# Optimization experiments

Hardware: AMD Instinct MI355X
Metric: run time of the kernel (lower is better)

## Reference

```python
import jax, jax.numpy as jnp
import numpy as np

NUM_HEADS = 12


def setup_inputs() -> dict:
    key = jax.random.key(0)
    k1, k2, k3 = jax.random.split(key, 3)
    B, S, D = 8, 1024, 768
    x = jax.random.normal(k1, (B, S, D), dtype=jnp.float32)
    # Linear weights, torch convention [out_features, in_features], small init
    w_qkv = jax.random.normal(k2, (3 * D, D), dtype=jnp.float32) * 0.02
    b_qkv = jnp.zeros((3 * D,), dtype=jnp.float32)
    w_proj = jax.random.normal(k3, (D, D), dtype=jnp.float32) * 0.02
    b_proj = jnp.zeros((D,), dtype=jnp.float32)
    return {"x": x, "w_qkv": w_qkv, "b_qkv": b_qkv, "w_proj": w_proj, "b_proj": b_proj}


def reference(x, w_qkv, b_qkv, w_proj, b_proj):
    B, S, D = x.shape
    H = NUM_HEADS
    hd = D // H
    qkv = x @ w_qkv.T + b_qkv                      # [B, S, 3D]
    qkv = qkv.reshape(B, S, 3, H, hd).transpose(2, 0, 3, 1, 4)  # [3, B, H, S, hd]
    q, k, v = qkv[0], qkv[1], qkv[2]
    # NOTE: source computes self.scale but never applies it -> unscaled QK^T
    weights = jnp.einsum('bhqd,bhkd->bhqk', q, k)  # [B, H, S, S]
    attn = jax.nn.softmax(weights, axis=-1)        # dropout = 0 (eval)
    out = jnp.einsum('bhqk,bhkd->bhqd', attn, v)   # [B, H, S, hd]
    out = out.transpose(0, 2, 1, 3).reshape(B, S, D)
    return out @ w_proj.T + b_proj
```

## Files before the change

kernel.cpp:

```cpp
#include <hip/hip_runtime.h>


typedef short bf16x8 __attribute__((ext_vector_type(8)));
typedef float f32x4  __attribute__((ext_vector_type(4)));

#define MFMA16(a, b, c) __builtin_amdgcn_mfma_f32_16x16x32_bf16((a), (b), (c), 0, 0, 0)

__device__ __forceinline__ unsigned short f2bf(float f) {
    union { float f; unsigned int u; } v; v.f = f;
    unsigned int u = v.u;
    return (unsigned short)((u + 0x7fffu + ((u >> 16) & 1u)) >> 16);
}

__device__ __forceinline__ unsigned int cvt2(float x, float y) {
#if __has_builtin(__builtin_amdgcn_cvt_pk_bf16_f32)
    auto v = __builtin_amdgcn_cvt_pk_bf16_f32(x, y);
    unsigned int b; __builtin_memcpy(&b, &v, 4); return b;
#else
    return (unsigned int)f2bf(x) | ((unsigned int)f2bf(y) << 16);
#endif
}

__device__ __forceinline__ void gl2lds16(const unsigned short* g, unsigned short* l) {
    __builtin_amdgcn_global_load_lds(
        (const unsigned int __attribute__((address_space(1)))*)g,
        (unsigned int __attribute__((address_space(3)))*)l,
        16, 0, 0);
}

__global__ void cvt3_kernel(const float* __restrict__ x,
                            const float* __restrict__ wq,
                            const float* __restrict__ wp,
                            unsigned short* __restrict__ xb,
                            unsigned short* __restrict__ wqb,
                            unsigned short* __restrict__ wpb) {
    int i = blockIdx.x * 256 + threadIdx.x;
    const float* s; unsigned short* d; int off;
    if (i < 1572864)      { s = x;  d = xb;  off = i; }
    else if (i < 2015232) { s = wq; d = wqb; off = i - 1572864; }
    else                  { s = wp; d = wpb; off = i - 2015232; }
    float4 v = ((const float4*)s)[off];
    ushort4 o;
    o.x = f2bf(v.x); o.y = f2bf(v.y); o.z = f2bf(v.z); o.w = f2bf(v.w);
    ((ushort4*)d)[off] = o;
}

__global__ __launch_bounds__(512, 4) void gemm_qkv(
    const unsigned short* __restrict__ A,
    const unsigned short* __restrict__ Bm,
    const float* __restrict__ bias,
    unsigned short* __restrict__ Qo,
    unsigned short* __restrict__ Ko,
    unsigned short* __restrict__ Vto) {
    const int K = 768;
    __shared__ __align__(16) unsigned short smem[16384];
    unsigned short* const As0 = smem;
    unsigned short* const As1 = smem + 4096;
    unsigned short* const Bs0 = smem + 8192;
    unsigned short* const Bs1 = smem + 12288;
    const int tid = threadIdx.x;
    const int wave = tid >> 6, lane = tid & 63;
    const int quad = lane >> 4, l16 = lane & 15;
    const int wm = (wave >> 1) * 32, wn = (wave & 1) * 64;
    const int tileM = blockIdx.x * 128, tileN = blockIdx.y * 128;

    f32x4 zero4 = {0.f, 0.f, 0.f, 0.f};
    f32x4 acc[2][4];
#pragma unroll
    for (int i = 0; i < 2; ++i)
#pragma unroll
        for (int j = 0; j < 4; ++j) acc[i][j] = zero4;

    const int sr = tid >> 2, sc = tid & 3;
    const unsigned short* Ag = A + (size_t)(tileM + sr) * K + sc * 8;
    const unsigned short* Bg = Bm + (size_t)(tileN + sr) * K + sc * 8;
    const int sdst = wave << 9;

    auto compute = [&](const unsigned short* Ar, const unsigned short* Br) {
        bf16x8 af[2], bfr[4];
#pragma unroll
        for (int t = 0; t < 2; ++t)
            af[t] = *(const bf16x8*)(Ar + (wm + t * 16 + l16) * 32 + quad * 8);
#pragma unroll
        for (int t = 0; t < 4; ++t)
            bfr[t] = *(const bf16x8*)(Br + (wn + t * 16 + l16) * 32 + quad * 8);
#pragma unroll
        for (int tm = 0; tm < 2; ++tm)
#pragma unroll
            for (int tn = 0; tn < 4; ++tn)
                acc[tm][tn] = MFMA16(af[tm], bfr[tn], acc[tm][tn]);
    };

    gl2lds16(Ag, As0 + sdst);
    gl2lds16(Bg, Bs0 + sdst);
    for (int it = 0; it < 24; it += 2) {
        __syncthreads();
        {
            int k1 = (it + 1) << 5;
            gl2lds16(Ag + k1, As1 + sdst);
            gl2lds16(Bg + k1, Bs1 + sdst);
        }
        compute(As0, Bs0);
        __syncthreads();
        if (it + 2 < 24) {
            int k2 = (it + 2) << 5;
            gl2lds16(Ag + k2, As0 + sdst);
            gl2lds16(Bg + k2, Bs0 + sdst);
        }
        compute(As1, Bs1);
    }

    const int t = blockIdx.y / 6;
    if (t < 2) {
        const float scale = (t == 0) ? 1.44269504f : 1.0f;
        unsigned short* dst = (t == 0) ? Qo : Ko;
        const int nb = tileN - t * 768 + wn;
#pragma unroll
        for (int tm = 0; tm < 2; ++tm) {
#pragma unroll
            for (int tn = 0; tn < 4; ++tn) {
                int nl = nb + tn * 16 + l16;
                float bv = bias[tileN + wn + tn * 16 + l16];
#pragma unroll
                for (int r = 0; r < 4; ++r) {
                    int m = tileM + wm + tm * 16 + quad * 4 + r;
                    dst[(size_t)m * 768 + nl] = f2bf((acc[tm][tn][r] + bv) * scale);
                }
            }
        }
    } else {
        const int b = tileM >> 10, srow = tileM & 1023;
#pragma unroll
        for (int h2 = 0; h2 < 2; ++h2) {
            __syncthreads();
            if ((wave & 1) == h2) {
#pragma unroll
                for (int tn = 0; tn < 4; ++tn) {
                    int dl = tn * 16 + l16;
                    float bv = bias[tileN + h2 * 64 + dl];
#pragma unroll
                    for (int tm = 0; tm < 2; ++tm) {
                        int mb = wm + tm * 16 + quad * 4;
                        uint2 pk;
                        pk.x = cvt2(acc[tm][tn][0] + bv, acc[tm][tn][1] + bv);
                        pk.y = cvt2(acc[tm][tn][2] + bv, acc[tm][tn][3] + bv);
                        *(uint2*)(smem + dl * 136 + mb) = pk;
                    }
                }
            }
            __syncthreads();
#pragma unroll
            for (int pass = 0; pass < 2; ++pass) {
                int dl = pass * 32 + (tid >> 4), soff = (tid & 15) * 8;
                bf16x8 row = *(const bf16x8*)(smem + dl * 136 + soff);
                int rem = tileN + h2 * 64 + dl - 1536;
                int h = rem >> 6, d = rem & 63;
                *(bf16x8*)(Vto + (((size_t)b * 12 + h) * 64 + d) * 1024 + srow + soff) = row;
            }
        }
    }
}

__global__ __launch_bounds__(256) void attn_kernel(
    const unsigned short* __restrict__ Q,
    const unsigned short* __restrict__ Kg,
    const unsigned short* __restrict__ Vt,
    unsigned short* __restrict__ O) {
    __shared__ __align__(16) unsigned short smem[24576];
    unsigned short* Ps = smem;

    const int tid = threadIdx.x;
    const int wave = tid >> 6, lane = tid & 63;
    const int quad = lane >> 4, l16 = lane & 15;
    const int s4 = l16 & 3;
    const int bh = blockIdx.x;
    const int qt = blockIdx.y;
    const int b = bh / 12, h = bh - b * 12;

    const unsigned short* Qb = Q  + ((size_t)b * 1024 + qt * 128) * 768 + h * 64;
    const unsigned short* Kb = Kg + (size_t)b * 1024 * 768 + h * 64;
    const unsigned short* Vb = Vt + (size_t)bh * 64 * 1024;

    auto stageKV = [&](int kv0, int buf) {
        int r = tid >> 2, c = tid & 3;
        const unsigned short* gk = Kb + (size_t)(kv0 + r) * 768 + c * 8;
        const unsigned short* gv = Vb + (size_t)r * 1024 + kv0 + c * 8;
        unsigned short* Kd = smem + 8192 + buf * 4096;
        unsigned short* Vd = smem + 16384 + buf * 4096;
        int dst = (wave << 6) * 8;
        gl2lds16(gk,      Kd + dst);
        gl2lds16(gk + 32, Kd + 2048 + dst);
        gl2lds16(gv,      Vd + dst);
        gl2lds16(gv + 32, Vd + 2048 + dst);
    };

#pragma unroll
    for (int i = 0; i < 2; ++i) {
        int s = tid + (i << 8);
        int r = s >> 2, c = s & 3;
        const unsigned short* gq = Qb + (size_t)r * 768 + c * 8;
        int dst = ((wave << 6) + (i << 8)) * 8;
        gl2lds16(gq,      smem + dst);
        gl2lds16(gq + 32, smem + 4096 + dst);
    }
    stageKV(0, 0);
    __syncthreads();
    bf16x8 qf[2][2];
#pragma unroll
    for (int ks = 0; ks < 2; ++ks)
#pragma unroll
        for (int tq = 0; tq < 2; ++tq)
            qf[ks][tq] = *(const bf16x8*)(smem + ks * 4096 +
                                          (wave * 32 + tq * 16 + l16) * 32 + quad * 8);
    __syncthreads();

    f32x4 zero4 = {0.f, 0.f, 0.f, 0.f};
    f32x4 oacc[2][4];
    float rsum[2] = {0.f, 0.f};
#pragma unroll
    for (int tm = 0; tm < 2; ++tm)
#pragma unroll
        for (int tv = 0; tv < 4; ++tv) oacc[tm][tv] = zero4;

    for (int it = 0; it < 16; ++it) {
        if (it + 1 < 16) stageKV((it + 1) << 6, (it + 1) & 1);
        const unsigned short* Kr = smem + 8192 + (it & 1) * 4096;
        const unsigned short* Vr = smem + 16384 + (it & 1) * 4096;

        f32x4 st[4][2];
#pragma unroll
        for (int tk = 0; tk < 4; ++tk)
#pragma unroll
            for (int tq = 0; tq < 2; ++tq) st[tk][tq] = zero4;
#pragma unroll
        for (int ks = 0; ks < 2; ++ks) {
            bf16x8 kf[4];
#pragma unroll
            for (int tk = 0; tk < 4; ++tk)
                kf[tk] = *(const bf16x8*)(Kr + ks * 2048 + (tk * 16 + l16) * 32 + quad * 8);
#pragma unroll
            for (int tk = 0; tk < 4; ++tk)
#pragma unroll
                for (int tq = 0; tq < 2; ++tq)
                    st[tk][tq] = MFMA16(kf[tk], qf[ks][tq], st[tk][tq]);
        }

#pragma unroll
        for (int tq = 0; tq < 2; ++tq) {
            unsigned short* prp = Ps + (wave * 32 + tq * 16 + l16) * 64 + quad * 4;
#pragma unroll
            for (int tk = 0; tk < 4; ++tk) {
                float e0 = __builtin_amdgcn_exp2f(st[tk][tq][0]);
                float e1 = __builtin_amdgcn_exp2f(st[tk][tq][1]);
                float e2 = __builtin_amdgcn_exp2f(st[tk][tq][2]);
                float e3 = __builtin_amdgcn_exp2f(st[tk][tq][3]);
                rsum[tq] += (e0 + e1) + (e2 + e3);
                uint2 pk;
                pk.x = cvt2(e0, e1);
                pk.y = cvt2(e2, e3);
                *(uint2*)(prp + ((tk ^ s4) << 4)) = pk;
            }
        }

#pragma unroll
        for (int ks2 = 0; ks2 < 2; ++ks2) {
            bf16x8 ap[2], bv[4];
            int colswz = ((ks2 << 5) + (quad << 3)) ^ (s4 << 4);
#pragma unroll
            for (int tm = 0; tm < 2; ++tm)
                ap[tm] = *(const bf16x8*)(Ps + (wave * 32 + tm * 16 + l16) * 64 + colswz);
#pragma unroll
            for (int tv = 0; tv < 4; ++tv)
                bv[tv] = *(const bf16x8*)(Vr + ks2 * 2048 + (tv * 16 + l16) * 32 + quad * 8);
#pragma unroll
            for (int tm = 0; tm < 2; ++tm)
#pragma unroll
                for (int tv = 0; tv < 4; ++tv)
                    oacc[tm][tv] = MFMA16(ap[tm], bv[tv], oacc[tm][tv]);
        }
        __syncthreads();
    }

#pragma unroll
    for (int tq = 0; tq < 2; ++tq) {
        rsum[tq] += __shfl_xor(rsum[tq], 16, 64);
        rsum[tq] += __shfl_xor(rsum[tq], 32, 64);
    }
    float* sums = (float*)smem;
    if (quad == 0) {
        sums[wave * 32 + l16]      = rsum[0];
        sums[wave * 32 + 16 + l16] = rsum[1];
    }
    __syncthreads();

#pragma unroll
    for (int tm = 0; tm < 2; ++tm) {
        f32x4 inv;
#pragma unroll
        for (int r = 0; r < 4; ++r)
            inv[r] = 1.0f / sums[wave * 32 + tm * 16 + quad * 4 + r];
#pragma unroll
        for (int tv = 0; tv < 4; ++tv)
#pragma unroll
            for (int r = 0; r < 4; ++r) {
                int srow = qt * 128 + wave * 32 + tm * 16 + quad * 4 + r;
                int col = h * 64 + tv * 16 + l16;
                O[((size_t)b * 1024 + srow) * 768 + col] = f2bf(oacc[tm][tv][r] * inv[r]);
            }
    }
}

__global__ __launch_bounds__(512, 4) void gemm_proj(
    const unsigned short* __restrict__ A,
    const unsigned short* __restrict__ Bm,
    const float* __restrict__ bias,
    float* __restrict__ out) {
    const int K = 768;
    __shared__ __align__(16) unsigned short smem[16384];
    unsigned short* const As0 = smem;
    unsigned short* const As1 = smem + 4096;
    unsigned short* const Bs0 = smem + 8192;
    unsigned short* const Bs1 = smem + 12288;
    const int tid = threadIdx.x;
    const int wave = tid >> 6, lane = tid & 63;
    const int quad = lane >> 4, l16 = lane & 15;
    const int wm = (wave >> 1) * 32, wn = (wave & 1) * 64;
    const int tileM = blockIdx.x * 128, tileN = blockIdx.y * 128;

    f32x4 zero4 = {0.f, 0.f, 0.f, 0.f};
    f32x4 acc[2][4];
#pragma unroll
    for (int i = 0; i < 2; ++i)
#pragma unroll
        for (int j = 0; j < 4; ++j) acc[i][j] = zero4;

    const int sr = tid >> 2, sc = tid & 3;
    const unsigned short* Ag = A + (size_t)(tileM + sr) * K + sc * 8;
    const unsigned short* Bg = Bm + (size_t)(tileN + sr) * K + sc * 8;
    const int sdst = wave << 9;

    auto compute = [&](const unsigned short* Ar, const unsigned short* Br) {
        bf16x8 af[2], bfr[4];
#pragma unroll
        for (int t = 0; t < 2; ++t)
            af[t] = *(const bf16x8*)(Ar + (wm + t * 16 + l16) * 32 + quad * 8);
#pragma unroll
        for (int t = 0; t < 4; ++t)
            bfr[t] = *(const bf16x8*)(Br + (wn + t * 16 + l16) * 32 + quad * 8);
#pragma unroll
        for (int tm = 0; tm < 2; ++tm)
#pragma unroll
            for (int tn = 0; tn < 4; ++tn)
                acc[tm][tn] = MFMA16(af[tm], bfr[tn], acc[tm][tn]);
    };

    gl2lds16(Ag, As0 + sdst);
    gl2lds16(Bg, Bs0 + sdst);
    for (int it = 0; it < 24; it += 2) {
        __syncthreads();
        {
            int k1 = (it + 1) << 5;
            gl2lds16(Ag + k1, As1 + sdst);
            gl2lds16(Bg + k1, Bs1 + sdst);
        }
        compute(As0, Bs0);
        __syncthreads();
        if (it + 2 < 24) {
            int k2 = (it + 2) << 5;
            gl2lds16(Ag + k2, As0 + sdst);
            gl2lds16(Bg + k2, Bs0 + sdst);
        }
        compute(As1, Bs1);
    }

#pragma unroll
    for (int tm = 0; tm < 2; ++tm) {
#pragma unroll
        for (int tn = 0; tn < 4; ++tn) {
            int n = tileN + wn + tn * 16 + l16;
            float bv = bias[n];
#pragma unroll
            for (int r = 0; r < 4; ++r) {
                int m = tileM + wm + tm * 16 + quad * 4 + r;
                out[(size_t)m * 768 + n] = acc[tm][tn][r] + bv;
            }
        }
    }
}

extern "C" void kernel_launch(void* const* d_in, const int* in_sizes, int n_in,
                              void* d_out, int out_size, void* d_ws, size_t ws_size,
                              hipStream_t stream) {
    (void)in_sizes; (void)n_in; (void)out_size; (void)ws_size;
    const float* x      = (const float*)d_in[0];
    const float* w_qkv  = (const float*)d_in[1];
    const float* b_qkv  = (const float*)d_in[2];
    const float* w_proj = (const float*)d_in[3];
    const float* b_proj = (const float*)d_in[4];
    float* out = (float*)d_out;

    char* ws = (char*)d_ws;
    unsigned short* xb     = (unsigned short*)(ws + 0);
    unsigned short* wqkvb  = (unsigned short*)(ws + 12582912);
    unsigned short* wprojb = (unsigned short*)(ws + 16121856);
    unsigned short* Qw     = (unsigned short*)(ws + 17301504);
    unsigned short* Kw     = (unsigned short*)(ws + 29884416);
    unsigned short* Vtw    = (unsigned short*)(ws + 42467328);

    cvt3_kernel<<<8448, 256, 0, stream>>>(x, w_qkv, w_proj, xb, wqkvb, wprojb);
    gemm_qkv<<<dim3(64, 18), 512, 0, stream>>>(xb, wqkvb, b_qkv, Qw, Kw, Vtw);
    attn_kernel<<<dim3(96, 8), 256, 0, stream>>>(Qw, Kw, Vtw, xb);
    gemm_proj<<<dim3(64, 6), 512, 0, stream>>>(xb, wprojb, b_proj, out);
}
```

Before: 187.0 us.

## Halve attention query tile to 64 rows and use MFMA-fragment-ordered LDS layout

```diff
diff --git a/kernel.cpp b/kernel.cpp
--- a/kernel.cpp
+++ b/kernel.cpp
@@ -161,153 +161,115 @@
     }
 }
 
-__global__ __launch_bounds__(256) void attn_kernel(
+__global__ __launch_bounds__(256, 4) void attn_kernel(
     const unsigned short* __restrict__ Q,
     const unsigned short* __restrict__ Kg,
     const unsigned short* __restrict__ Vt,
     unsigned short* __restrict__ O) {
-    __shared__ __align__(16) unsigned short smem[24576];
-    unsigned short* Ps = smem;
+    __shared__ __align__(16) unsigned short smem[20480];
 
     const int tid = threadIdx.x;
     const int wave = tid >> 6, lane = tid & 63;
     const int quad = lane >> 4, l16 = lane & 15;
-    const int s4 = l16 & 3;
     const int bh = blockIdx.x;
     const int qt = blockIdx.y;
     const int b = bh / 12, h = bh - b * 12;
 
-    const unsigned short* Qb = Q  + ((size_t)b * 1024 + qt * 128) * 768 + h * 64;
+    const unsigned short* Qb = Q  + ((size_t)b * 1024 + qt * 64) * 768 + h * 64;
     const unsigned short* Kb = Kg + (size_t)b * 1024 * 768 + h * 64;
     const unsigned short* Vb = Vt + (size_t)bh * 64 * 1024;
 
+    const int c0 = wave * 2, c1 = c0 + 1;
+    const unsigned short* gk0 = Kb + (size_t)((c0 & 3) * 16 + l16) * 768 + (c0 >> 2) * 32 + quad * 8;
+    const unsigned short* gk1 = Kb + (size_t)((c1 & 3) * 16 + l16) * 768 + (c1 >> 2) * 32 + quad * 8;
+    const unsigned short* gv0 = Vb + (size_t)((c0 & 3) * 16 + l16) * 1024 + (c0 >> 2) * 32 + quad * 8;
+    const unsigned short* gv1 = Vb + (size_t)((c1 & 3) * 16 + l16) * 1024 + (c1 >> 2) * 32 + quad * 8;
+
     auto stageKV = [&](int kv0, int buf) {
-        int r = tid >> 2, c = tid & 3;
-        const unsigned short* gk = Kb + (size_t)(kv0 + r) * 768 + c * 8;
-        const unsigned short* gv = Vb + (size_t)r * 1024 + kv0 + c * 8;
-        unsigned short* Kd = smem + 8192 + buf * 4096;
-        unsigned short* Vd = smem + 16384 + buf * 4096;
-        int dst = (wave << 6) * 8;
-        gl2lds16(gk,      Kd + dst);
-        gl2lds16(gk + 32, Kd + 2048 + dst);
-        gl2lds16(gv,      Vd + dst);
-        gl2lds16(gv + 32, Vd + 2048 + dst);
+        unsigned short* Kd = smem + 4096 + buf * 4096;
+        unsigned short* Vd = smem + 12288 + buf * 4096;
+        gl2lds16(gk0 + (size_t)kv0 * 768, Kd + c0 * 512);
+        gl2lds16(gk1 + (size_t)kv0 * 768, Kd + c1 * 512);
+        gl2lds16(gv0 + kv0, Vd + c0 * 512);
+        gl2lds16(gv1 + kv0, Vd + c1 * 512);
     };
 
-#pragma unroll
-    for (int i = 0; i < 2; ++i) {
-        int s = tid + (i << 8);
-        int r = s >> 2, c = s & 3;
-        const unsigned short* gq = Qb + (size_t)r * 768 + c * 8;
-        int dst = ((wave << 6) + (i << 8)) * 8;
-        gl2lds16(gq,      smem + dst);
-        gl2lds16(gq + 32, smem + 4096 + dst);
-    }
+    gl2lds16(Qb + (size_t)(wave * 16 + l16) * 768 + quad * 8,      smem + c0 * 512);
+    gl2lds16(Qb + (size_t)(wave * 16 + l16) * 768 + 32 + quad * 8, smem + c1 * 512);
     stageKV(0, 0);
     __syncthreads();
-    bf16x8 qf[2][2];
-#pragma unroll
-    for (int ks = 0; ks < 2; ++ks)
-#pragma unroll
-        for (int tq = 0; tq < 2; ++tq)
-            qf[ks][tq] = *(const bf16x8*)(smem + ks * 4096 +
-                                          (wave * 32 + tq * 16 + l16) * 32 + quad * 8);
-    __syncthreads();
-
+    bf16x8 qf[2];
+    qf[0] = *(const bf16x8*)(smem + c0 * 512 + lane * 8);
+    qf[1] = *(const bf16x8*)(smem + c1 * 512 + lane * 8);
+
+    unsigned short* Pw = smem + wave * 1024;
     f32x4 zero4 = {0.f, 0.f, 0.f, 0.f};
-    f32x4 oacc[2][4];
-    float rsum[2] = {0.f, 0.f};
-#pragma unroll
-    for (int tm = 0; tm < 2; ++tm)
-#pragma unroll
-        for (int tv = 0; tv < 4; ++tv) oacc[tm][tv] = zero4;
+    f32x4 oacc[4];
+    float rsum = 0.f;
+#pragma unroll
+    for (int tv = 0; tv < 4; ++tv) oacc[tv] = zero4;
 
     for (int it = 0; it < 16; ++it) {
         if (it + 1 < 16) stageKV((it + 1) << 6, (it + 1) & 1);
-        const unsigned short* Kr = smem + 8192 + (it & 1) * 4096;
-        const unsigned short* Vr = smem + 16384 + (it & 1) * 4096;
-
-        f32x4 st[4][2];
-#pragma unroll
-        for (int tk = 0; tk < 4; ++tk)
-#pragma unroll
-            for (int tq = 0; tq < 2; ++tq) st[tk][tq] = zero4;
+        const unsigned short* Kr = smem + 4096 + (it & 1) * 4096;
+        const unsigned short* Vr = smem + 12288 + (it & 1) * 4096;
+
+        f32x4 st[4];
+#pragma unroll
+        for (int tk = 0; tk < 4; ++tk) st[tk] = zero4;
 #pragma unroll
         for (int ks = 0; ks < 2; ++ks) {
             bf16x8 kf[4];
 #pragma unroll
             for (int tk = 0; tk < 4; ++tk)
-                kf[tk] = *(const bf16x8*)(Kr + ks * 2048 + (tk * 16 + l16) * 32 + quad * 8);
+                kf[tk] = *(const bf16x8*)(Kr + (ks * 4 + tk) * 512 + lane * 8);
 #pragma unroll
             for (int tk = 0; tk < 4; ++tk)
-#pragma unroll
-                for (int tq = 0; tq < 2; ++tq)
-                    st[tk][tq] = MFMA16(kf[tk], qf[ks][tq], st[tk][tq]);
-        }
-
-#pragma unroll
-        for (int tq = 0; tq < 2; ++tq) {
-            unsigned short* prp = Ps + (wave * 32 + tq * 16 + l16) * 64 + quad * 4;
-#pragma unroll
-            for (int tk = 0; tk < 4; ++tk) {
-                float e0 = __builtin_amdgcn_exp2f(st[tk][tq][0]);
-                float e1 = __builtin_amdgcn_exp2f(st[tk][tq][1]);
-                float e2 = __builtin_amdgcn_exp2f(st[tk][tq][2]);
-                float e3 = __builtin_amdgcn_exp2f(st[tk][tq][3]);
-                rsum[tq] += (e0 + e1) + (e2 + e3);
-                uint2 pk;
-                pk.x = cvt2(e0, e1);
-                pk.y = cvt2(e2, e3);
-                *(uint2*)(prp + ((tk ^ s4) << 4)) = pk;
-            }
+                st[tk] = MFMA16(kf[tk], qf[ks], st[tk]);
+        }
+
+#pragma unroll
+        for (int tk = 0; tk < 4; ++tk) {
+            float e0 = __builtin_amdgcn_exp2f(st[tk][0]);
+            float e1 = __builtin_amdgcn_exp2f(st[tk][1]);
+            float e2 = __builtin_amdgcn_exp2f(st[tk][2]);
+            float e3 = __builtin_amdgcn_exp2f(st[tk][3]);
+            rsum += (e0 + e1) + (e2 + e3);
+            uint2 pk;
+            pk.x = cvt2(e0, e1);
+            pk.y = cvt2(e2, e3);
+            *(uint2*)(Pw + (tk * 2 + (quad >> 1)) * 128 + l16 * 8 + (quad & 1) * 4) = pk;
         }
 
 #pragma unroll
         for (int ks2 = 0; ks2 < 2; ++ks2) {
-            bf16x8 ap[2], bv[4];
-            int colswz = ((ks2 << 5) + (quad << 3)) ^ (s4 << 4);
-#pragma unroll
-            for (int tm = 0; tm < 2; ++tm)
-                ap[tm] = *(const bf16x8*)(Ps + (wave * 32 + tm * 16 + l16) * 64 + colswz);
+            bf16x8 ap = *(const bf16x8*)(Pw + ks2 * 512 + lane * 8);
+            bf16x8 bv[4];
 #pragma unroll
             for (int tv = 0; tv < 4; ++tv)
-                bv[tv] = *(const bf16x8*)(Vr + ks2 * 2048 + (tv * 16 + l16) * 32 + quad * 8);
-#pragma unroll
-            for (int tm = 0; tm < 2; ++tm)
-#pragma unroll
-                for (int tv = 0; tv < 4; ++tv)
-                    oacc[tm][tv] = MFMA16(ap[tm], bv[tv], oacc[tm][tv]);
-        }
-        __syncthreads();
-    }
-
-#pragma unroll
-    for (int tq = 0; tq < 2; ++tq) {
-        rsum[tq] += __shfl_xor(rsum[tq], 16, 64);
-        rsum[tq] += __shfl_xor(rsum[tq], 32, 64);
-    }
-    float* sums = (float*)smem;
-    if (quad == 0) {
-        sums[wave * 32 + l16]      = rsum[0];
-        sums[wave * 32 + 16 + l16] = rsum[1];
-    }
-    __syncthreads();
-
-#pragma unroll
-    for (int tm = 0; tm < 2; ++tm) {
-        f32x4 inv;
-#pragma unroll
-        for (int r = 0; r < 4; ++r)
-            inv[r] = 1.0f / sums[wave * 32 + tm * 16 + quad * 4 + r];
-#pragma unroll
-        for (int tv = 0; tv < 4; ++tv)
-#pragma unroll
-            for (int r = 0; r < 4; ++r) {
-                int srow = qt * 128 + wave * 32 + tm * 16 + quad * 4 + r;
-                int col = h * 64 + tv * 16 + l16;
-                O[((size_t)b * 1024 + srow) * 768 + col] = f2bf(oacc[tm][tv][r] * inv[r]);
-            }
-    }
+                bv[tv] = *(const bf16x8*)(Vr + (ks2 * 4 + tv) * 512 + lane * 8);
+#pragma unroll
+            for (int tv = 0; tv < 4; ++tv)
+                oacc[tv] = MFMA16(ap, bv[tv], oacc[tv]);
+        }
+        __syncthreads();
+    }
+
+    rsum += __shfl_xor(rsum, 16, 64);
+    rsum += __shfl_xor(rsum, 32, 64);
+    float inv[4];
+#pragma unroll
+    for (int r = 0; r < 4; ++r)
+        inv[r] = 1.0f / __shfl(rsum, quad * 4 + r, 64);
+
+#pragma unroll
+    for (int tv = 0; tv < 4; ++tv)
+#pragma unroll
+        for (int r = 0; r < 4; ++r) {
+            int srow = qt * 64 + wave * 16 + quad * 4 + r;
+            int col = h * 64 + tv * 16 + l16;
+            O[((size_t)b * 1024 + srow) * 768 + col] = f2bf(oacc[tv][r] * inv[r]);
+        }
 }
 
 __global__ __launch_bounds__(512, 4) void gemm_proj(
@@ -409,6 +371,6 @@
 
     cvt3_kernel<<<8448, 256, 0, stream>>>(x, w_qkv, w_proj, xb, wqkvb, wprojb);
     gemm_qkv<<<dim3(64, 18), 512, 0, stream>>>(xb, wqkvb, b_qkv, Qw, Kw, Vtw);
-    attn_kernel<<<dim3(96, 8), 256, 0, stream>>>(Qw, Kw, Vtw, xb);
+    attn_kernel<<<dim3(96, 16), 256, 0, stream>>>(Qw, Kw, Vtw, xb);
     gemm_proj<<<dim3(64, 6), 512, 0, stream>>>(xb, wprojb, b_proj, out);
 }
```

Result: slower. 196.3 us (+5.0%).
